# Optimization experiments

Measured on AMD Instinct MI355X. Metric: run time of the kernel, lower is better.

Reference implementation:

```python
import jax, jax.numpy as jnp
import numpy as np
import math

N, E, R = 50000, 800000, 32
DIN = 128
H, D = 8, 16          # num_heads, head_dim; H*D == out_ent_feats == 128
HOP = 5
ALPHA = 0.1
EPS = 1e-5


def layer_norm(x, g, b):
    m = jnp.mean(x, axis=-1, keepdims=True)
    v = jnp.mean((x - m) ** 2, axis=-1, keepdims=True)
    return (x - m) * jax.lax.rsqrt(v + EPS) * g + b


def segment_softmax(e, dst, num_nodes):
    # e: [E, H] scores, softmax over incoming edges of each dst node
    m = jax.ops.segment_max(e, dst, num_segments=num_nodes)      # [N, H]
    ex = jnp.exp(e - m[dst])
    s = jax.ops.segment_sum(ex, dst, num_segments=num_nodes)     # [N, H]
    return ex / s[dst]


def setup_inputs() -> dict:
    key = jax.random.key(0)
    ks = jax.random.split(key, 12)
    gain = 0.02  # small init scale (small_init_gain-style)
    ent_feat = jax.random.normal(ks[0], (N, DIN), dtype=jnp.float32)
    rel_feat = jax.random.normal(ks[1], (R, DIN), dtype=jnp.float32)
    src = jax.random.randint(ks[2], (E,), 0, N, dtype=jnp.int32)
    # guarantee every node has in-degree >= 1 (DGL raises otherwise)
    dst_rand = jax.random.randint(ks[3], (E - N,), 0, N, dtype=jnp.int32)
    dst = jnp.concatenate([jnp.arange(N, dtype=jnp.int32), dst_rand])
    rid = jax.random.randint(ks[4], (E,), 0, R, dtype=jnp.int32)
    W_head = jax.random.normal(ks[5], (DIN, H * D), dtype=jnp.float32) * gain
    W_tail = jax.random.normal(ks[6], (DIN, H * D), dtype=jnp.float32) * gain
    W_ent = jax.random.normal(ks[7], (DIN, H * D), dtype=jnp.float32) * gain
    W_rel = jax.random.normal(ks[8], (DIN, H * D), dtype=jnp.float32) * gain
    attn_r = jax.random.normal(ks[9], (1, H, D), dtype=jnp.float32) * gain
    W1 = jax.random.normal(ks[10], (H * D, 4 * H * D), dtype=jnp.float32) * gain
    W2 = jax.random.normal(ks[11], (4 * H * D, H * D), dtype=jnp.float32) * gain
    return dict(
        ent_feat=ent_feat, rel_feat=rel_feat, src=src, dst=dst, rid=rid,
        W_head=W_head, W_tail=W_tail, W_ent=W_ent, W_rel=W_rel, attn_r=attn_r,
        ln_ent_g=jnp.ones((DIN,), jnp.float32), ln_ent_b=jnp.zeros((DIN,), jnp.float32),
        ln_rel_g=jnp.ones((DIN,), jnp.float32), ln_rel_b=jnp.zeros((DIN,), jnp.float32),
        ff_ln_g=jnp.ones((H * D,), jnp.float32), ff_ln_b=jnp.zeros((H * D,), jnp.float32),
        W1=W1, b1=jnp.zeros((4 * H * D,), jnp.float32),
        W2=W2, b2=jnp.zeros((H * D,), jnp.float32),
    )


def _forward(ent_feat, rel_feat, src, dst, rid,
             W_head, W_tail, W_ent, W_rel, attn_r,
             ln_ent_g, ln_ent_b, ln_rel_g, ln_rel_b, ff_ln_g, ff_ln_b,
             W1, b1, W2, b2):
    n = ent_feat.shape[0]
    x = layer_norm(ent_feat, ln_ent_g, ln_ent_b)
    feat_head = (x @ W_head).reshape(n, H, D)
    feat_tail = (x @ W_tail).reshape(n, H, D)
    feat_ent = (x @ W_ent).reshape(n, H, D)

    # per-edge dot-product attention score: u_dot_v('eh','et')
    e = jnp.sum(feat_head[src] * feat_tail[dst], axis=-1)          # [E, H]

    r = layer_norm(rel_feat, ln_rel_g, ln_rel_b)
    feat_rel = (r @ W_rel).reshape(R, H, D)
    er = jnp.sum(feat_rel * attn_r, axis=-1)                       # [R, H]
    e = e * er[rid]                                                # [E, H]

    # e_mul_v with log_in = log(in_degree) of dst node
    deg = jax.ops.segment_sum(jnp.ones((e.shape[0],), e.dtype), dst, num_segments=n)
    log_in = jnp.log(jnp.maximum(deg, 1.0))                        # [N]
    e = e * log_in[dst][:, None] / math.sqrt(D)

    a = segment_softmax(e, dst, n)                                 # [E, H]

    # PPR diffusion: feat <- (1-alpha) * A^T feat + alpha * feat_0
    feat = feat_ent
    for _ in range(HOP):
        msg = feat[src] * a[:, :, None]                            # [E, H, D]
        agg = jax.ops.segment_sum(msg, dst, num_segments=n)        # [N, H, D]
        feat = (1.0 - ALPHA) * agg + ALPHA * feat_ent

    # residual (Identity: in_ent_feats == out_ent_feats)
    rst = feat + ent_feat.reshape(n, H, D)
    rst = rst.reshape(n, H * D)

    h = layer_norm(rst, ff_ln_g, ff_ln_b)
    ff = jax.nn.relu(h @ W1 + b1) @ W2 + b2
    return ff + rst


def reference(ent_feat, rel_feat, src, dst, rid,
              W_head, W_tail, W_ent, W_rel, attn_r,
              ln_ent_g, ln_ent_b, ln_rel_g, ln_rel_b, ff_ln_g, ff_ln_b,
              W1, b1, W2, b2):
    return _forward(ent_feat, rel_feat, src, dst, rid,
                    W_head, W_tail, W_ent, W_rel, attn_r,
                    ln_ent_g, ln_ent_b, ln_rel_g, ln_rel_b, ff_ln_g, ff_ln_b,
                    W1, b1, W2, b2)
```

## Files before the change

kernel.cpp:

```cpp
#include <hip/hip_runtime.h>
#include <hip/hip_bf16.h>

#define N_NODES 50000
#define N_EDGES 800000
#define N_REL 32
#define DIN 128
#define NH 8
#define HD 16
#define FF_HID 512
#define EPS_LN 1e-5f
#define NBUCK 8
#define BDIV 6250
#define BCAP 114688

typedef __attribute__((ext_vector_type(8))) short bf16x8;
typedef __attribute__((ext_vector_type(4))) float f32x4;
typedef __attribute__((ext_vector_type(2))) float f32x2;
typedef unsigned short ushort_t;
typedef unsigned int uint_t;

static __device__ __forceinline__ unsigned short f2bf(float f) {
    union { float f; unsigned u; } v; v.f = f;
    unsigned r = (v.u + 0x7fffu + ((v.u >> 16) & 1u)) >> 16;
    return (unsigned short)r;
}
static __device__ __forceinline__ float bf2f(unsigned u16) {
    union { unsigned u; float f; } v; v.u = u16 << 16; return v.f;
}
static __device__ __forceinline__ unsigned char f2fp8(float f) {
    return (unsigned char)(__builtin_amdgcn_cvt_pk_fp8_f32(f, f, 0, false) & 0xff);
}
static __device__ __forceinline__ uint_t f2fp8x2(float x0, float x1) {
    return (__builtin_amdgcn_cvt_pk_fp8_f32(x0, x1, 0, false) & 0xffffu);
}
static __device__ __forceinline__ void fp8x4_to_f32(uint_t w, float* o) {
    f32x2 lo = __builtin_amdgcn_cvt_pk_f32_fp8(w, false);
    f32x2 hi = __builtin_amdgcn_cvt_pk_f32_fp8(w, true);
    o[0] = lo.x; o[1] = lo.y; o[2] = hi.x; o[3] = hi.y;
}

static __device__ __forceinline__ void pack_dev(const float* __restrict__ W,
                                                short* __restrict__ out, int K, int Ncols,
                                                int idx) {
    int KT = K >> 5;
    int l = idx & 63;
    int tile = idx >> 6;
    int kt = tile & (KT - 1);
    int ct = tile / KT;
    int c = ct * 16 + (l & 15);
    int k0 = kt * 32 + ((l >> 4) * 8);
    bf16x8 v;
#pragma unroll
    for (int j = 0; j < 8; j++) v[j] = (short)f2bf(W[(size_t)(k0 + j) * Ncols + c]);
    *(bf16x8*)(out + (size_t)idx * 8) = v;
}

#define C0_BIN 512
__global__ __launch_bounds__(256) void combo0_kernel(
    const int* __restrict__ src, const int* __restrict__ dst, const int* __restrict__ rid,
    int* __restrict__ gcnt, int* __restrict__ bdst, int* __restrict__ bpay,
    const float* __restrict__ W1, short* __restrict__ W1p, const float* __restrict__ W2,
    short* __restrict__ W2p, const float* __restrict__ Wh, short* __restrict__ Whp,
    const float* __restrict__ Wt, short* __restrict__ Wtp, const float* __restrict__ We,
    short* __restrict__ Wep, const float* __restrict__ rel_feat,
    const float* __restrict__ gr, const float* __restrict__ br,
    const float* __restrict__ W_rel, const float* __restrict__ attn_r,
    float* __restrict__ er) {
    __shared__ float red[128];
    __shared__ float xsr[128];
    __shared__ float prod[128];
    __shared__ int cnt[NBUCK];
    __shared__ int sbase[NBUCK];
    int b = blockIdx.x, tid = threadIdx.x;
    if (b < C0_BIN) {
        const int chunk = (N_EDGES + C0_BIN - 1) / C0_BIN;
        int i0 = b * chunk;
        int i1 = min(i0 + chunk, N_EDGES);
        int rounds = (i1 - i0 + 255) >> 8;
        for (int r = 0; r < rounds; r++) {
            int i = i0 + (r << 8) + tid;
            if (tid < NBUCK) cnt[tid] = 0;
            __syncthreads();
            int d = 0, b8 = 0, rank = 0, py = 0;
            bool v = i < i1;
            if (v) {
                d = dst[i];
                b8 = d / BDIV;
                py = src[i] | (rid[i] << 16);
                rank = atomicAdd(&cnt[b8], 1);
            }
            __syncthreads();
            if (tid < NBUCK) sbase[tid] = atomicAdd(&gcnt[tid], cnt[tid]);
            __syncthreads();
            if (v) {
                size_t pos = (size_t)b8 * BCAP + sbase[b8] + rank;
                bdst[pos] = d;
                bpay[pos] = py;
            }
            __syncthreads();
        }
    } else if (b < C0_BIN + 32) {
        pack_dev(W1, W1p, DIN, FF_HID, (b - C0_BIN) * 256 + tid);
    } else if (b < C0_BIN + 64) {
        pack_dev(W2, W2p, FF_HID, DIN, (b - C0_BIN - 32) * 256 + tid);
    } else if (b < C0_BIN + 72) {
        pack_dev(Wh, Whp, DIN, DIN, (b - C0_BIN - 64) * 256 + tid);
    } else if (b < C0_BIN + 80) {
        pack_dev(Wt, Wtp, DIN, DIN, (b - C0_BIN - 72) * 256 + tid);
    } else if (b < C0_BIN + 88) {
        pack_dev(We, Wep, DIN, DIN, (b - C0_BIN - 80) * 256 + tid);
    } else {
        int r = b - (C0_BIN + 88);
        float x = 0.f;
        if (tid < 128) {
            x = rel_feat[r * DIN + tid];
            red[tid] = x;
        }
        __syncthreads();
        for (int off = 64; off > 0; off >>= 1) {
            if (tid < off) red[tid] += red[tid + off];
            __syncthreads();
        }
        float mean = red[0] * (1.f / DIN);
        __syncthreads();
        if (tid < 128) red[tid] = x * x;
        __syncthreads();
        for (int off = 64; off > 0; off >>= 1) {
            if (tid < off) red[tid] += red[tid + off];
            __syncthreads();
        }
        float var = red[0] * (1.f / DIN) - mean * mean;
        float rs = rsqrtf(var + EPS_LN);
        if (tid < 128) xsr[tid] = (x - mean) * rs * gr[tid] + br[tid];
        __syncthreads();
        if (tid < 128) {
            float acc = 0.f;
            for (int k = 0; k < DIN; k++) acc += xsr[k] * W_rel[k * DIN + tid];
            prod[tid] = acc * attn_r[tid];
        }
        __syncthreads();
        if (tid < NH) {
            float s = 0.f;
            for (int d = 0; d < HD; d++) s += prod[tid * HD + d];
            er[r * NH + tid] = s;
        }
    }
}

#define C_HIST 1024
__global__ __launch_bounds__(256) void combo_mid_kernel(
    const int* __restrict__ bdst, const int* __restrict__ gcnt, int* __restrict__ deg,
    const float* __restrict__ ent, const float* __restrict__ g, const float* __restrict__ b,
    const short* __restrict__ Whp, const short* __restrict__ Wtp,
    const short* __restrict__ Wep, unsigned char* __restrict__ hent,
    ushort_t* __restrict__ tail_bf) {
    __shared__ float xs[32][128];
    __shared__ short hsb[32][136];
    int blk = blockIdx.x, tid = threadIdx.x;
    if (blk < C_HIST) {
        int b8 = blk & 7, sub = blk >> 3;
        int cnt = gcnt[b8];
        int chunk = (cnt + 127) >> 7;
        int i0 = sub * chunk;
        int i1 = min(i0 + chunk, cnt);
        const int* bp = bdst + (size_t)b8 * BCAP;
        for (int i = i0 + tid; i < i1; i += 256) atomicAdd(&deg[bp[i]], 1);
        return;
    }
    int base = (blk - C_HIST) * 32;
    {
        int c = tid & 127, rb = tid >> 7;
#pragma unroll
        for (int j = 0; j < 16; j++) {
            int r = j * 2 + rb;
            int row = base + r;
            xs[r][c] = (row < N_NODES) ? ent[(size_t)row * DIN + c] : 0.f;
        }
    }
    __syncthreads();
    int wave = tid >> 6, lane = tid & 63;
    {
        float g0 = g[lane], g1 = g[lane + 64], bb0 = b[lane], bb1 = b[lane + 64];
        for (int r = wave * 8; r < wave * 8 + 8; r++) {
            float x0 = xs[r][lane], x1 = xs[r][lane + 64];
            float s1 = x0 + x1, s2 = x0 * x0 + x1 * x1;
            for (int m = 1; m < 64; m <<= 1) {
                s1 += __shfl_xor(s1, m);
                s2 += __shfl_xor(s2, m);
            }
            float mean = s1 * (1.f / DIN);
            float var = s2 * (1.f / DIN) - mean * mean;
            float rs = rsqrtf(var + EPS_LN);
            hsb[r][lane] = (short)f2bf((x0 - mean) * rs * g0 + bb0);
            hsb[r][lane + 64] = (short)f2bf((x1 - mean) * rs * g1 + bb1);
        }
    }
    __syncthreads();
    bf16x8 a[2][4];
#pragma unroll
    for (int rt = 0; rt < 2; rt++)
#pragma unroll
        for (int kt = 0; kt < 4; kt++)
            a[rt][kt] = *(const bf16x8*)&hsb[rt * 16 + (lane & 15)][kt * 32 + (lane >> 4) * 8];
#pragma unroll
    for (int m = 0; m < 3; m++) {
        const bf16x8* bp = (m == 0)   ? (const bf16x8*)Whp
                           : (m == 1) ? (const bf16x8*)Wtp
                                      : (const bf16x8*)Wep;
#pragma unroll
        for (int c2 = 0; c2 < 2; c2++) {
            int ct = wave * 2 + c2;
            f32x4 acc0 = {0.f, 0.f, 0.f, 0.f}, acc1 = {0.f, 0.f, 0.f, 0.f};
#pragma unroll
            for (int kt = 0; kt < 4; kt++) {
                bf16x8 bf = bp[(ct * 4 + kt) * 64 + lane];
                acc0 = __builtin_amdgcn_mfma_f32_16x16x32_bf16(a[0][kt], bf, acc0, 0, 0, 0);
                acc1 = __builtin_amdgcn_mfma_f32_16x16x32_bf16(a[1][kt], bf, acc1, 0, 0, 0);
            }
            int col = ct * 16 + (lane & 15);
            int h = col >> 4, k = col & 15;
            int r0 = (lane >> 4) * 4;
#pragma unroll
            for (int j = 0; j < 4; j++) {
                int row0 = base + r0 + j, row1 = base + 16 + r0 + j;
                if (m == 0) {
                    if (row0 < N_NODES) hent[(size_t)row0 * 256 + h * 32 + k] = f2fp8(acc0[j]);
                    if (row1 < N_NODES) hent[(size_t)row1 * 256 + h * 32 + k] = f2fp8(acc1[j]);
                } else if (m == 1) {
                    if (row0 < N_NODES) tail_bf[(size_t)row0 * DIN + col] = f2bf(acc0[j]);
                    if (row1 < N_NODES) tail_bf[(size_t)row1 * DIN + col] = f2bf(acc1[j]);
                } else {
                    if (row0 < N_NODES)
                        hent[(size_t)row0 * 256 + h * 32 + 16 + k] = f2fp8(acc0[j]);
                    if (row1 < N_NODES)
                        hent[(size_t)row1 * 256 + h * 32 + 16 + k] = f2fp8(acc1[j]);
                }
            }
        }
    }
}

__global__ __launch_bounds__(256) void scan2_kernel(const int* __restrict__ deg,
                                                    int* __restrict__ row_off, int n) {
    __shared__ int lscan[256];
    __shared__ int ws4[4];
    int blk = blockIdx.x, tid = threadIdx.x;
    int start = blk * 256;
    int partial = 0;
    for (int i = tid; i < start; i += 256) partial += deg[i];
    for (int m = 32; m > 0; m >>= 1) partial += __shfl_down(partial, m);
    int wid = tid >> 6, lane = tid & 63;
    if (lane == 0) ws4[wid] = partial;
    __syncthreads();
    int sbase = ws4[0] + ws4[1] + ws4[2] + ws4[3];
    int i = start + tid;
    int v = (i < n) ? deg[i] : 0;
    lscan[tid] = v;
    __syncthreads();
    for (int off = 1; off < 256; off <<= 1) {
        int t = (tid >= off) ? lscan[tid - off] : 0;
        __syncthreads();
        lscan[tid] += t;
        __syncthreads();
    }
    if (i < n) row_off[i] = sbase + lscan[tid] - v;
    if (i == n - 1) row_off[n] = sbase + lscan[tid];
}

__global__ __launch_bounds__(256) void scatter_kernel(
    const int* __restrict__ bdst, const int* __restrict__ bpay,
    const int* __restrict__ gcnt, const int* __restrict__ row_off,
    int* __restrict__ cursor, int* __restrict__ sr_perm) {
    int blk = blockIdx.x, tid = threadIdx.x;
    int b8 = blk & 7, sub = blk >> 3;
    int cnt = gcnt[b8];
    int chunk = (cnt + 127) >> 7;
    int i0 = sub * chunk;
    int i1 = min(i0 + chunk, cnt);
    const int* bd = bdst + (size_t)b8 * BCAP;
    const int* bpp = bpay + (size_t)b8 * BCAP;
    for (int i = i0 + tid; i < i1; i += 256) {
        int d = bd[i];
        int p = row_off[d] + atomicAdd(&cursor[d], 1);
        sr_perm[p] = bpp[i];
    }
}

__global__ __launch_bounds__(256) void score_hop_kernel(
    const unsigned char* __restrict__ hent, const ushort_t* __restrict__ tail_bf,
    const float* __restrict__ er, const int* __restrict__ row_off,
    const int* __restrict__ sr_perm, ushort_t* __restrict__ a_bf,
    float* __restrict__ inv9, unsigned char* __restrict__ fout) {
    int wid = threadIdx.x >> 6;
    int u = blockIdx.x * 4 + wid;
    int lane = threadIdx.x & 63;
    int h = lane & 7, esub = lane >> 3;
    int p0 = row_off[u], p1 = row_off[u + 1];
    int deg = p1 - p0;
    float scale = logf((float)(deg > 0 ? deg : 1)) * 0.25f;
    float t[16];
    {
        const uint_t* tp = (const uint_t*)(tail_bf + (size_t)u * DIN + h * HD);
#pragma unroll
        for (int i = 0; i < 8; i++) {
            uint_t w = tp[i];
            t[2 * i] = bf2f(w & 0xffffu);
            t[2 * i + 1] = bf2f(w >> 16);
        }
    }
    float ssum = 0.f;
    float acc[16];
#pragma unroll
    for (int k = 0; k < 16; k++) acc[k] = 0.f;
    for (int p = p0 + esub; p < p1; p += 8) {
        int v = sr_perm[p];
        int s = v & 0xffff;
        int rr = v >> 16;
        const uint4* hp = (const uint4*)(hent + (size_t)s * 256 + h * 32);
        uint4 hw = hp[0];
        uint4 ew = hp[1];
        float hv[16], ev[16];
        fp8x4_to_f32(hw.x, hv + 0); fp8x4_to_f32(hw.y, hv + 4);
        fp8x4_to_f32(hw.z, hv + 8); fp8x4_to_f32(hw.w, hv + 12);
        fp8x4_to_f32(ew.x, ev + 0); fp8x4_to_f32(ew.y, ev + 4);
        fp8x4_to_f32(ew.z, ev + 8); fp8x4_to_f32(ew.w, ev + 12);
        float dot = 0.f;
#pragma unroll
        for (int k = 0; k < 16; k++) dot += t[k] * hv[k];
        float e = dot * er[rr * NH + h] * scale;
        float sx = expf(e);
        a_bf[(size_t)p * NH + h] = f2bf(sx);
        ssum += sx;
#pragma unroll
        for (int k = 0; k < 16; k++) acc[k] += sx * ev[k];
    }
    ssum += __shfl_xor(ssum, 8);
    ssum += __shfl_xor(ssum, 16);
    ssum += __shfl_xor(ssum, 32);
#pragma unroll
    for (int k = 0; k < 16; k++) {
        acc[k] += __shfl_xor(acc[k], 8);
        acc[k] += __shfl_xor(acc[k], 16);
        acc[k] += __shfl_xor(acc[k], 32);
    }
    if (esub == 0) {
        float iv = 0.9f / ssum;
        inv9[(size_t)u * NH + h] = iv;
        const uint4 eu = *(const uint4*)(hent + (size_t)u * 256 + h * 32 + 16);
        float e0[16];
        fp8x4_to_f32(eu.x, e0 + 0); fp8x4_to_f32(eu.y, e0 + 4);
        fp8x4_to_f32(eu.z, e0 + 8); fp8x4_to_f32(eu.w, e0 + 12);
        float x[16];
#pragma unroll
        for (int k = 0; k < 16; k++) x[k] = iv * acc[k] + 0.1f * e0[k];
        uint4 ov;
        ov.x = f2fp8x2(x[0], x[1]) | (f2fp8x2(x[2], x[3]) << 16);
        ov.y = f2fp8x2(x[4], x[5]) | (f2fp8x2(x[6], x[7]) << 16);
        ov.z = f2fp8x2(x[8], x[9]) | (f2fp8x2(x[10], x[11]) << 16);
        ov.w = f2fp8x2(x[12], x[13]) | (f2fp8x2(x[14], x[15]) << 16);
        *(uint4*)(fout + (size_t)u * DIN + h * HD) = ov;
    }
}

template <bool OUT_BF>
__global__ __launch_bounds__(256) void diffuse4_kernel(
    const unsigned char* __restrict__ fin8, const unsigned char* __restrict__ hent,
    const ushort_t* __restrict__ a_bf, const int* __restrict__ sr_perm,
    const int* __restrict__ row_off, const float* __restrict__ inv9,
    void* __restrict__ fout) {
    int wid = threadIdx.x >> 6;
    int u = blockIdx.x * 4 + wid;
    int lane = threadIdx.x & 63;
    int c = lane & 15;
    int g = lane >> 4;
    int hh = c >> 1;
    int p0 = row_off[u], p1 = row_off[u + 1];
    float acc[8];
#pragma unroll
    for (int j = 0; j < 8; j++) acc[j] = 0.f;
    for (int p = p0; p < p1; p += 4) {
        int pe = p + g;
        bool valid = pe < p1;
        int pc = valid ? pe : (p1 - 1);
        int s = sr_perm[pc] & 0xffff;
        float a = valid ? bf2f(a_bf[(size_t)pc * NH + hh]) : 0.f;
        uint2 w = *(const uint2*)(fin8 + (size_t)s * DIN + 8 * c);
        float v[8];
        fp8x4_to_f32(w.x, v + 0);
        fp8x4_to_f32(w.y, v + 4);
#pragma unroll
        for (int j = 0; j < 8; j++) acc[j] += a * v[j];
    }
#pragma unroll
    for (int j = 0; j < 8; j++) {
        acc[j] += __shfl_xor(acc[j], 16);
        acc[j] += __shfl_xor(acc[j], 32);
    }
    if (g == 0) {
        float iv = inv9[(size_t)u * NH + hh];
        uint2 ew = *(const uint2*)(hent + (size_t)u * 256 + hh * 32 + 16 + (c & 1) * 8);
        float e0[8];
        fp8x4_to_f32(ew.x, e0 + 0);
        fp8x4_to_f32(ew.y, e0 + 4);
        float x[8];
#pragma unroll
        for (int j = 0; j < 8; j++) x[j] = iv * acc[j] + 0.1f * e0[j];
        size_t o = (size_t)u * DIN + 8 * c;
        if (OUT_BF) {
            uint4 ov;
            ov.x = (uint_t)f2bf(x[0]) | ((uint_t)f2bf(x[1]) << 16);
            ov.y = (uint_t)f2bf(x[2]) | ((uint_t)f2bf(x[3]) << 16);
            ov.z = (uint_t)f2bf(x[4]) | ((uint_t)f2bf(x[5]) << 16);
            ov.w = (uint_t)f2bf(x[6]) | ((uint_t)f2bf(x[7]) << 16);
            *(uint4*)((ushort_t*)fout + o) = ov;
        } else {
            uint2 ov;
            ov.x = f2fp8x2(x[0], x[1]) | (f2fp8x2(x[2], x[3]) << 16);
            ov.y = f2fp8x2(x[4], x[5]) | (f2fp8x2(x[6], x[7]) << 16);
            *(uint2*)((unsigned char*)fout + o) = ov;
        }
    }
}

static __device__ __forceinline__ int hid_idx(int row, int col) {
    return row * 512 + ((((col >> 3) & 63) ^ (row & 7)) << 3) + (col & 7);
}
__global__ __launch_bounds__(256) void ffn_mfma_kernel(
    const ushort_t* __restrict__ feat, const float* __restrict__ ent0,
    const float* __restrict__ g, const float* __restrict__ b,
    const short* __restrict__ W1p, const float* __restrict__ b1,
    const short* __restrict__ W2p, const float* __restrict__ b2,
    float* __restrict__ out) {
    __shared__ ushort_t rst_bf[16][136];
    __shared__ short hs[16][136];
    __shared__ short hid[16 * 512];
    int tid = threadIdx.x;
    int base = blockIdx.x * 16;
    int wave = tid >> 6, lane = tid & 63;
    {
        int c = tid & 127, rb = tid >> 7;
#pragma unroll
        for (int j = 0; j < 8; j++) {
            int r = j * 2 + rb;
            int row = base + r;
            float v = 0.f;
            if (row < N_NODES) {
                size_t idx = (size_t)row * DIN + c;
                v = bf2f(feat[idx]) + ent0[idx];
            }
            rst_bf[r][c] = f2bf(v);
        }
    }
    __syncthreads();
    {
        float g0 = g[lane], g1 = g[lane + 64], bb0 = b[lane], bb1 = b[lane + 64];
        for (int r = wave * 4; r < wave * 4 + 4; r++) {
            float x0 = bf2f(rst_bf[r][lane]), x1 = bf2f(rst_bf[r][lane + 64]);
            float s1 = x0 + x1, s2 = x0 * x0 + x1 * x1;
            for (int m = 1; m < 64; m <<= 1) {
                s1 += __shfl_xor(s1, m);
                s2 += __shfl_xor(s2, m);
            }
            float mean = s1 * (1.f / DIN);
            float var = s2 * (1.f / DIN) - mean * mean;
            float rs = rsqrtf(var + EPS_LN);
            hs[r][lane] = (short)f2bf((x0 - mean) * rs * g0 + bb0);
            hs[r][lane + 64] = (short)f2bf((x1 - mean) * rs * g1 + bb1);
        }
    }
    __syncthreads();
    {
        bf16x8 a[4];
#pragma unroll
        for (int kt = 0; kt < 4; kt++)
            a[kt] = *(const bf16x8*)&hs[lane & 15][kt * 32 + (lane >> 4) * 8];
        const bf16x8* bp = (const bf16x8*)W1p;
        for (int cti = 0; cti < 8; cti++) {
            int ct = wave * 8 + cti;
            f32x4 acc0 = {0.f, 0.f, 0.f, 0.f};
#pragma unroll
            for (int kt = 0; kt < 4; kt++) {
                bf16x8 bf = bp[(ct * 4 + kt) * 64 + lane];
                acc0 = __builtin_amdgcn_mfma_f32_16x16x32_bf16(a[kt], bf, acc0, 0, 0, 0);
            }
            int col = ct * 16 + (lane & 15);
            float bv = b1[col];
            int r0 = (lane >> 4) * 4;
#pragma unroll
            for (int j = 0; j < 4; j++)
                hid[hid_idx(r0 + j, col)] = (short)f2bf(fmaxf(acc0[j] + bv, 0.f));
        }
    }
    __syncthreads();
    {
        f32x4 acc[2] = {{0.f, 0.f, 0.f, 0.f}, {0.f, 0.f, 0.f, 0.f}};
        const bf16x8* bp2 = (const bf16x8*)W2p;
        for (int kt = 0; kt < 16; kt++) {
            int col8 = kt * 32 + (lane >> 4) * 8;
            bf16x8 a0 = *(const bf16x8*)&hid[hid_idx(lane & 15, col8)];
#pragma unroll
            for (int c2 = 0; c2 < 2; c2++) {
                int ct = wave * 2 + c2;
                bf16x8 bf = bp2[(ct * 16 + kt) * 64 + lane];
                acc[c2] = __builtin_amdgcn_mfma_f32_16x16x32_bf16(a0, bf, acc[c2], 0, 0, 0);
            }
        }
#pragma unroll
        for (int c2 = 0; c2 < 2; c2++) {
            int col = (wave * 2 + c2) * 16 + (lane & 15);
            float bv = b2[col];
            int r0 = (lane >> 4) * 4;
#pragma unroll
            for (int j = 0; j < 4; j++) {
                int row = base + r0 + j;
                if (row < N_NODES)
                    out[(size_t)row * DIN + col] = acc[c2][j] + bv + bf2f(rst_bf[r0 + j][col]);
            }
        }
    }
}

extern "C" void kernel_launch(void* const* d_in, const int* in_sizes, int n_in,
                              void* d_out, int out_size, void* d_ws, size_t ws_size,
                              hipStream_t stream) {
    const float* ent_feat = (const float*)d_in[0];
    const float* rel_feat = (const float*)d_in[1];
    const int* src = (const int*)d_in[2];
    const int* dst = (const int*)d_in[3];
    const int* rid = (const int*)d_in[4];
    const float* W_head = (const float*)d_in[5];
    const float* W_tail = (const float*)d_in[6];
    const float* W_ent = (const float*)d_in[7];
    const float* W_rel = (const float*)d_in[8];
    const float* attn_r = (const float*)d_in[9];
    const float* ln_ent_g = (const float*)d_in[10];
    const float* ln_ent_b = (const float*)d_in[11];
    const float* ln_rel_g = (const float*)d_in[12];
    const float* ln_rel_b = (const float*)d_in[13];
    const float* ff_ln_g = (const float*)d_in[14];
    const float* ff_ln_b = (const float*)d_in[15];
    const float* W1 = (const float*)d_in[16];
    const float* b1 = (const float*)d_in[17];
    const float* W2 = (const float*)d_in[18];
    const float* b2 = (const float*)d_in[19];
    float* out = (float*)d_out;

    const int N = N_NODES, E = N_EDGES;

    char* cur = (char*)d_ws;
    auto alloc = [&](size_t bytes, size_t align) -> void* {
        uintptr_t p = (uintptr_t)cur;
        p = (p + align - 1) & ~(uintptr_t)(align - 1);
        cur = (char*)(p + bytes);
        return (void*)p;
    };
    ushort_t* tail_bf = (ushort_t*)alloc((size_t)N * DIN * 2, 16);
    unsigned char* hent = (unsigned char*)alloc((size_t)N * 256, 16);
    unsigned char* f8A = (unsigned char*)alloc((size_t)N * DIN, 16);
    unsigned char* f8B = (unsigned char*)alloc((size_t)N * DIN, 16);
    int* bdst = (int*)alloc((size_t)NBUCK * BCAP * 4, 16);
    int* bpay = (int*)alloc((size_t)NBUCK * BCAP * 4, 16);
    int* sr_perm = (int*)alloc((size_t)E * 4, 16);
    int* row_off = (int*)alloc((size_t)(N + 1) * 4, 16);
    int* deg = (int*)alloc(((size_t)2 * N + NBUCK) * 4, 16);
    int* cursor = deg + N;
    int* gcnt = deg + 2 * N;
    float* er = (float*)alloc((size_t)N_REL * NH * 4, 16);
    float* inv9 = (float*)alloc((size_t)N * NH * 4, 16);
    short* W1p = (short*)alloc((size_t)DIN * FF_HID * 2, 16);
    short* W2p = (short*)alloc((size_t)FF_HID * DIN * 2, 16);
    short* Whp = (short*)alloc((size_t)DIN * DIN * 2, 16);
    short* Wtp = (short*)alloc((size_t)DIN * DIN * 2, 16);
    short* Wep = (short*)alloc((size_t)DIN * DIN * 2, 16);
    ushort_t* a_fit = (ushort_t*)alloc((size_t)E * NH * 2, 16);
    bool a_in_ws = ((size_t)(cur - (char*)d_ws) <= ws_size);
    ushort_t* a_bf = a_in_ws ? a_fit : (ushort_t*)d_out;

    hipMemsetAsync(deg, 0, sizeof(int) * ((size_t)2 * N + NBUCK), stream);
    combo0_kernel<<<632, 256, 0, stream>>>(src, dst, rid, gcnt, bdst, bpay, W1, W1p, W2,
                                           W2p, W_head, Whp, W_tail, Wtp, W_ent, Wep,
                                           rel_feat, ln_rel_g, ln_rel_b, W_rel, attn_r,
                                           er);
    int nblk32 = (N + 31) / 32;
    combo_mid_kernel<<<C_HIST + nblk32, 256, 0, stream>>>(
        bdst, gcnt, deg, ent_feat, ln_ent_g, ln_ent_b, Whp, Wtp, Wep, hent, tail_bf);
    scan2_kernel<<<(N + 255) / 256, 256, 0, stream>>>(deg, row_off, N);
    scatter_kernel<<<1024, 256, 0, stream>>>(bdst, bpay, gcnt, row_off, cursor, sr_perm);
    score_hop_kernel<<<N / 4, 256, 0, stream>>>(hent, tail_bf, er, row_off, sr_perm,
                                                a_bf, inv9, f8A);
    diffuse4_kernel<false><<<N / 4, 256, 0, stream>>>(f8A, hent, a_bf, sr_perm, row_off,
                                                      inv9, f8B);
    diffuse4_kernel<false><<<N / 4, 256, 0, stream>>>(f8B, hent, a_bf, sr_perm, row_off,
                                                      inv9, f8A);
    diffuse4_kernel<false><<<N / 4, 256, 0, stream>>>(f8A, hent, a_bf, sr_perm, row_off,
                                                      inv9, f8B);
    diffuse4_kernel<true><<<N / 4, 256, 0, stream>>>(f8B, hent, a_bf, sr_perm, row_off,
                                                     inv9, tail_bf);
    int nblk16 = (N + 15) / 16;
    ffn_mfma_kernel<<<nblk16, 256, 0, stream>>>(tail_bf, ent_feat, ff_ln_g, ff_ln_b, W1p,
                                                b1, W2p, b2, out);
}
```

Measured before the change: 400.2 us.

## Use shared-memory degree histogram and fuse prefix scan into projection kernel

Degree counting moves out of the combined projection kernel into its own kernel with 64 blocks. Each block builds a bucket-local histogram in shared memory and flushes the nonzero bins to global memory with atomics, which cuts global atomic traffic. The degree scan, previously a separate kernel, now runs as the first 196 blocks of the projection kernel, removing one launch. The cost is an extra histogram launch with only 64 blocks, so little parallelism, and the shared-memory atomics may contend within a block.

```diff
diff --git a/kernel.cpp b/kernel.cpp
--- a/kernel.cpp
+++ b/kernel.cpp
@@ -147,9 +147,32 @@
     }
 }
 
-#define C_HIST 1024
+#define NHB 8
+__global__ __launch_bounds__(256) void hist2_kernel(const int* __restrict__ bdst,
+                                                    const int* __restrict__ gcnt,
+                                                    int* __restrict__ deg) {
+    __shared__ int lhist[BDIV];
+    int blk = blockIdx.x, tid = threadIdx.x;
+    int b8 = blk & 7, sub = blk >> 3;
+    for (int i = tid; i < BDIV; i += 256) lhist[i] = 0;
+    __syncthreads();
+    int cnt = gcnt[b8];
+    int chunk = (cnt + NHB - 1) / NHB;
+    int i0 = sub * chunk;
+    int i1 = min(i0 + chunk, cnt);
+    const int* bp = bdst + (size_t)b8 * BCAP;
+    int w0 = b8 * BDIV;
+    for (int i = i0 + tid; i < i1; i += 256) atomicAdd(&lhist[bp[i] - w0], 1);
+    __syncthreads();
+    for (int i = tid; i < BDIV; i += 256) {
+        int v = lhist[i];
+        if (v) atomicAdd(&deg[w0 + i], v);
+    }
+}
+
+#define NS_SCAN 196
 __global__ __launch_bounds__(256) void combo_mid_kernel(
-    const int* __restrict__ bdst, const int* __restrict__ gcnt, int* __restrict__ deg,
+    const int* __restrict__ deg, int* __restrict__ row_off,
     const float* __restrict__ ent, const float* __restrict__ g, const float* __restrict__ b,
     const short* __restrict__ Whp, const short* __restrict__ Wtp,
     const short* __restrict__ Wep, unsigned char* __restrict__ hent,
@@ -157,17 +180,33 @@
     __shared__ float xs[32][128];
     __shared__ short hsb[32][136];
     int blk = blockIdx.x, tid = threadIdx.x;
-    if (blk < C_HIST) {
-        int b8 = blk & 7, sub = blk >> 3;
-        int cnt = gcnt[b8];
-        int chunk = (cnt + 127) >> 7;
-        int i0 = sub * chunk;
-        int i1 = min(i0 + chunk, cnt);
-        const int* bp = bdst + (size_t)b8 * BCAP;
-        for (int i = i0 + tid; i < i1; i += 256) atomicAdd(&deg[bp[i]], 1);
+    if (blk < NS_SCAN) {
+        __shared__ int lscan[256];
+        __shared__ int ws4[4];
+        int n = N_NODES;
+        int start = blk * 256;
+        int partial = 0;
+        for (int i = tid; i < start; i += 256) partial += deg[i];
+        for (int m = 32; m > 0; m >>= 1) partial += __shfl_down(partial, m);
+        int wid = tid >> 6, lane = tid & 63;
+        if (lane == 0) ws4[wid] = partial;
+        __syncthreads();
+        int sbase = ws4[0] + ws4[1] + ws4[2] + ws4[3];
+        int i = start + tid;
+        int v = (i < n) ? deg[i] : 0;
+        lscan[tid] = v;
+        __syncthreads();
+        for (int off = 1; off < 256; off <<= 1) {
+            int t = (tid >= off) ? lscan[tid - off] : 0;
+            __syncthreads();
+            lscan[tid] += t;
+            __syncthreads();
+        }
+        if (i < n) row_off[i] = sbase + lscan[tid] - v;
+        if (i == n - 1) row_off[n] = sbase + lscan[tid];
         return;
     }
-    int base = (blk - C_HIST) * 32;
+    int base = (blk - NS_SCAN) * 32;
     {
         int c = tid & 127, rb = tid >> 7;
 #pragma unroll
@@ -238,33 +277,6 @@
             }
         }
     }
-}
-
-__global__ __launch_bounds__(256) void scan2_kernel(const int* __restrict__ deg,
-                                                    int* __restrict__ row_off, int n) {
-    __shared__ int lscan[256];
-    __shared__ int ws4[4];
-    int blk = blockIdx.x, tid = threadIdx.x;
-    int start = blk * 256;
-    int partial = 0;
-    for (int i = tid; i < start; i += 256) partial += deg[i];
-    for (int m = 32; m > 0; m >>= 1) partial += __shfl_down(partial, m);
-    int wid = tid >> 6, lane = tid & 63;
-    if (lane == 0) ws4[wid] = partial;
-    __syncthreads();
-    int sbase = ws4[0] + ws4[1] + ws4[2] + ws4[3];
-    int i = start + tid;
-    int v = (i < n) ? deg[i] : 0;
-    lscan[tid] = v;
-    __syncthreads();
-    for (int off = 1; off < 256; off <<= 1) {
-        int t = (tid >= off) ? lscan[tid - off] : 0;
-        __syncthreads();
-        lscan[tid] += t;
-        __syncthreads();
-    }
-    if (i < n) row_off[i] = sbase + lscan[tid] - v;
-    if (i == n - 1) row_off[n] = sbase + lscan[tid];
 }
 
 __global__ __launch_bounds__(256) void scatter_kernel(
@@ -581,10 +593,10 @@
                                            W2p, W_head, Whp, W_tail, Wtp, W_ent, Wep,
                                            rel_feat, ln_rel_g, ln_rel_b, W_rel, attn_r,
                                            er);
+    hist2_kernel<<<NBUCK * NHB, 256, 0, stream>>>(bdst, gcnt, deg);
     int nblk32 = (N + 31) / 32;
-    combo_mid_kernel<<<C_HIST + nblk32, 256, 0, stream>>>(
-        bdst, gcnt, deg, ent_feat, ln_ent_g, ln_ent_b, Whp, Wtp, Wep, hent, tail_bf);
-    scan2_kernel<<<(N + 255) / 256, 256, 0, stream>>>(deg, row_off, N);
+    combo_mid_kernel<<<NS_SCAN + nblk32, 256, 0, stream>>>(
+        deg, row_off, ent_feat, ln_ent_g, ln_ent_b, Whp, Wtp, Wep, hent, tail_bf);
     scatter_kernel<<<1024, 256, 0, stream>>>(bdst, bpay, gcnt, row_off, cursor, sr_perm);
     score_hop_kernel<<<N / 4, 256, 0, stream>>>(hent, tail_bf, er, row_off, sr_perm,
                                                 a_bf, inv9, f8A);
```

After: 364.1 us. 1.1x faster.
